# Kernel optimization log

Measured on AMD Instinct MI355X. Metric: run time of the kernel, lower is better.

## Reference

```python
import jax, jax.numpy as jnp
import numpy as np

NUM_HEADS = 12


def setup_inputs() -> dict:
    key = jax.random.key(0)
    k1, k2, k3, k4, k5 = jax.random.split(key, 5)
    B, N, C = 4, 1024, 768
    x = jax.random.normal(k1, (B, N, C), dtype=jnp.float32)
    y = jax.random.normal(k2, (B, N, C), dtype=jnp.float32)
    w_qkv = jax.random.normal(k3, (4 * C, C), dtype=jnp.float32) * 0.02
    w_proj = jax.random.normal(k4, (C, C), dtype=jnp.float32) * 0.02
    b_proj = jax.random.normal(k5, (C,), dtype=jnp.float32) * 0.02
    return {"x": x, "y": y, "w_qkv": w_qkv, "w_proj": w_proj, "b_proj": b_proj}


def reference(x, y, w_qkv, w_proj, b_proj):
    B, N, C = x.shape
    H = NUM_HEADS
    hd = C // H
    scale = hd ** (-0.5)

    def qkv4(t):
        # Linear(dim, 4*dim, bias=False): t @ W^T -> [B,N,4C] -> [4,B,H,N,hd]
        p = (t @ w_qkv.T).reshape(B, N, 4, H, hd).transpose(2, 0, 3, 1, 4)
        return p[0], p[1], p[2], p[3]

    qxo, qx, kx, vx = qkv4(x)
    qyo, qy, ky, _vy_from_y = qkv4(y)
    vy = vx  # faithful to source: vy = qkv[3] (from x), not qkv2[3]

    def attend(q, k, v, neg):
        s = jnp.einsum('bhnd,bhmd->bhnm', q, k) * scale
        a = jax.nn.softmax(-s if neg else s, axis=-1)
        o = jnp.einsum('bhnm,bhmd->bhnd', a, v)
        return o.transpose(0, 2, 1, 3).reshape(B, N, C)

    x_self = attend(qx, kx, vx, False)
    y_self = attend(qy, ky, vy, False)
    x_cross = attend(qyo, kx, vx, True)   # attnx = -(qyo @ kx^T)
    y_cross = attend(qxo, ky, vy, True)   # attny = -(qxo @ ky^T)

    out_x = (x_self + x_cross) @ w_proj.T + b_proj
    out_y = (y_self + y_cross) @ w_proj.T + b_proj
    return (out_x, out_y)
```

## Files before the change

kernel.cpp:

```cpp
#include <hip/hip_runtime.h>
#include <hip/hip_bf16.h>
#include <stdint.h>


#define BB 4
#define NN 1024
#define CC 768
#define HH 12
#define HD 64

typedef unsigned short u16;
typedef short short8 __attribute__((ext_vector_type(8)));
typedef float f32x4 __attribute__((ext_vector_type(4)));

extern "C" __device__ float __ocml_native_exp2_f32(float);

__device__ __forceinline__ u16 f2bf(float f) {
  unsigned int u = __float_as_uint(f);
  return (u16)((u + 0x7fffu + ((u >> 16) & 1u)) >> 16);
}

__device__ __forceinline__ void load_lds16(const u16* g, u16* l) {
  __builtin_amdgcn_global_load_lds((__attribute__((address_space(1))) const void*)g,
                                   (__attribute__((address_space(3))) void*)l, 16, 0, 0);
}

__global__ __launch_bounds__(256)
void cvt_bf16(const float* __restrict__ x, const float* __restrict__ y,
              const float* __restrict__ wq, const float* __restrict__ wp,
              u16* __restrict__ xb, u16* __restrict__ yb,
              u16* __restrict__ wqb, u16* __restrict__ wpb)
{
  const int seg = blockIdx.y;
  const float* src = seg == 0 ? x : (seg == 1 ? y : (seg == 2 ? wq : wp));
  u16* dst = seg == 0 ? xb : (seg == 1 ? yb : (seg == 2 ? wqb : wpb));
  const int n = (seg == 3) ? 768 * 768 : ((seg == 2) ? 3072 * 768 : 4096 * 768);
  const int i = (blockIdx.x * 256 + threadIdx.x) * 8;
  if (i >= n) return;
  float sc = 1.0f;
  if (seg == 2) {
    const int row = i / 768;
    sc = (row < 768) ? -0.18033688f : (row < 1536 ? 0.18033688f : 1.0f);
  }
  float4 a = *(const float4*)(src + i);
  float4 b = *(const float4*)(src + i + 4);
  ushort4 u0 = {f2bf(a.x * sc), f2bf(a.y * sc), f2bf(a.z * sc), f2bf(a.w * sc)};
  ushort4 u1 = {f2bf(b.x * sc), f2bf(b.y * sc), f2bf(b.z * sc), f2bf(b.w * sc)};
  *(ushort4*)(dst + i) = u0;
  *(ushort4*)(dst + i + 4) = u1;
}

__global__ __launch_bounds__(256)
void vtrans(const u16* __restrict__ qkvx, u16* __restrict__ VT)
{
  const int blk = blockIdx.x;
  const int xcd = blk & 7, slot = blk >> 3;
  const int bh = (slot >> 5) * 8 + xcd;
  const int kt = slot & 31;
  const int b = bh / HH, h = bh % HH;
  const int t = threadIdx.x;
  const int key = kt * 32 + (t >> 3), d0 = (t & 7) * 8;
  uint4 v = *(const uint4*)(qkvx + (size_t)(b * NN + key) * 3072 + 3 * CC + h * HD + d0);
  u16 e[8];
  *(uint4*)e = v;
#pragma unroll
  for (int i = 0; i < 8; i++)
    VT[(size_t)(bh * 64 + d0 + i) * 1024 + key] = e[i];
}

template<int NP, bool BF16OUT, bool BIAS>
__global__ __launch_bounds__(256)
void gemm_mfma(const u16* __restrict__ A0, const u16* __restrict__ A1,
               const u16* __restrict__ W, const float* __restrict__ bias,
               void* __restrict__ C0, void* __restrict__ C1)
{
  __shared__ u16 As[128 * 64];
  __shared__ u16 Bs[128 * 64];
  const u16* A = blockIdx.z ? A1 : A0;
  void* C = blockIdx.z ? C1 : C0;
  const int m0 = blockIdx.y * 128, n0 = blockIdx.x * 128;
  const int t = threadIdx.x, w = t >> 6, lane = t & 63;
  const int c = lane & 15, qq = lane >> 4;
  const int mq = (w >> 1) * 64, nq = (w & 1) * 64;

  const int lrow = lane >> 3;
  const int lchunk = (lane & 7) ^ lrow;
  size_t arow[4], brow[4];
#pragma unroll
  for (int i = 0; i < 4; i++) {
    const int r = (w * 4 + i) * 8 + lrow;
    arow[i] = (size_t)(m0 + r) * 768 + lchunk * 8;
    brow[i] = (size_t)(n0 + r) * 768 + lchunk * 8;
  }

  f32x4 acc[4][4] = {};
  for (int k0 = 0; k0 < 768; k0 += 64) {
    __syncthreads();
#pragma unroll
    for (int i = 0; i < 4; i++) {
      load_lds16(A + arow[i] + k0, As + (w * 4 + i) * 512);
      load_lds16(W + brow[i] + k0, Bs + (w * 4 + i) * 512);
    }
    __syncthreads();
#pragma unroll
    for (int s = 0; s < 2; s++) {
      const int swz = ((s * 4 + qq) ^ (c & 7)) * 8;
      short8 af[4], bf[4];
#pragma unroll
      for (int i = 0; i < 4; i++)
        af[i] = *(const short8*)&As[(mq + i * 16 + c) * 64 + swz];
#pragma unroll
      for (int j = 0; j < 4; j++)
        bf[j] = *(const short8*)&Bs[(nq + j * 16 + c) * 64 + swz];
#pragma unroll
      for (int i = 0; i < 4; i++)
#pragma unroll
        for (int j = 0; j < 4; j++)
          acc[i][j] = __builtin_amdgcn_mfma_f32_16x16x32_bf16(af[i], bf[j], acc[i][j], 0, 0, 0);
    }
  }
  float bj[4] = {0.f, 0.f, 0.f, 0.f};
  if (BIAS) {
#pragma unroll
    for (int j = 0; j < 4; j++) bj[j] = bias[n0 + nq + c + j * 16];
  }
#pragma unroll
  for (int i = 0; i < 4; i++)
#pragma unroll
    for (int r = 0; r < 4; r++) {
      const size_t row = (size_t)(m0 + mq + i * 16 + qq * 4 + r) * NP + n0 + nq + c;
      if (BF16OUT) {
#pragma unroll
        for (int j = 0; j < 4; j++)
          ((u16*)C)[row + j * 16] = f2bf(acc[i][j][r]);
      } else {
#pragma unroll
        for (int j = 0; j < 4; j++)
          ((float*)C)[row + j * 16] = acc[i][j][r] + bj[j];
      }
    }
}

__global__ __launch_bounds__(256, 4)
void attn_pair_mfma(const u16* __restrict__ qkvx, const u16* __restrict__ qkvy,
                    const u16* __restrict__ VT,
                    u16* __restrict__ sum_x, u16* __restrict__ sum_y)
{
  __shared__ __align__(16) u16 smem[17408];
  float (*Of)[68] = (float(*)[68])smem;

  const int blk = blockIdx.x;
  const int xcd = blk & 7, slot = blk >> 3;
  const int bh = (slot >> 5) * 8 + xcd;
  const int inner = slot & 31;
  const int qt = inner >> 1, pair = inner & 1;
  const int b = bh / HH, head = bh % HH;
  const u16* q1 = pair ? qkvy : qkvx;
  const u16* q2 = pair ? qkvx : qkvy;
  const u16* ks = pair ? qkvy : qkvx;
  u16* outp = pair ? sum_y : sum_x;

  const int t = threadIdx.x, w = t >> 6, lane = t & 63;
  const int c = lane & 15, qq = lane >> 4;

  short8 Qf[2][2];
  {
    const int qrow = qt * 64 + w * 16 + c;
    const u16* qs = q1 + (size_t)(b * NN + qrow) * 3072 + CC + head * HD + qq * 8;
    const u16* qc = q2 + (size_t)(b * NN + qrow) * 3072 + head * HD + qq * 8;
    Qf[0][0] = *(const short8*)qs;
    Qf[0][1] = *(const short8*)(qs + 32);
    Qf[1][0] = *(const short8*)qc;
    Qf[1][1] = *(const short8*)(qc + 32);
  }

  const u16* kbase = ks + (size_t)(b * NN) * 3072 + 2 * CC + head * HD;
  const u16* vtb = VT + (size_t)(bh * 64) * 1024;

  const int lr = lane >> 3;
  const int sc8 = ((lane & 7) ^ lr) * 8;

  u16* Pw = smem + 8192 + w * 2304;

  short8 ones;
#pragma unroll
  for (int i = 0; i < 8; i++) ones[i] = (short)0x3F80;

  f32x4 O[2][4] = {};
  f32x4 L[2] = {};

  const int cx = c & 7;
  const int koff0 = (qq ^ cx) * 8;
  const int koff1 = ((4 + qq) ^ cx) * 8;
  const int c6 = (6 * c) & 7;
  const int poff0 = ((qq + c6) & 7) * 8;
  const int poff1 = ((4 + qq + c6) & 7) * 8;

  for (int c16 = 0; c16 < 16; ++c16) {
    __syncthreads();
#pragma unroll
    for (int i = 0; i < 2; i++) {
      const int r = (2 * w + i) * 8 + lr;
      load_lds16(kbase + (size_t)(c16 * 64 + r) * 3072 + sc8,
                 smem + (2 * w + i) * 512);
      load_lds16(vtb + (size_t)r * 1024 + c16 * 64 + sc8,
                 smem + 4096 + (2 * w + i) * 512);
    }
    __syncthreads();

#pragma unroll
    for (int t4 = 0; t4 < 4; t4++) {
      const u16* kr = smem + (16 * t4 + c) * 64;
      short8 k0 = *(const short8*)(kr + koff0);
      short8 k1 = *(const short8*)(kr + koff1);
      const int l = 2 * t4 + (qq >> 1);
      const int base = c * 72 + (((l + c6) & 7) * 8) + 4 * (qq & 1);
#pragma unroll
      for (int s = 0; s < 2; s++) {
        f32x4 z = {0.f, 0.f, 0.f, 0.f};
        z = __builtin_amdgcn_mfma_f32_16x16x32_bf16(k0, Qf[s][0], z, 0, 0, 0);
        z = __builtin_amdgcn_mfma_f32_16x16x32_bf16(k1, Qf[s][1], z, 0, 0, 0);
        unsigned int u0 = __float_as_uint(__ocml_native_exp2_f32(z[0]));
        unsigned int u1 = __float_as_uint(__ocml_native_exp2_f32(z[1]));
        unsigned int u2 = __float_as_uint(__ocml_native_exp2_f32(z[2]));
        unsigned int u3 = __float_as_uint(__ocml_native_exp2_f32(z[3]));
        uint2 pk;
        pk.x = __builtin_amdgcn_perm(u1, u0, 0x07060302u);
        pk.y = __builtin_amdgcn_perm(u3, u2, 0x07060302u);
        *(uint2*)(Pw + s * 1152 + base) = pk;
      }
    }

    short8 pa[2][2];
#pragma unroll
    for (int s = 0; s < 2; s++) {
      const u16* pr = Pw + s * 1152 + c * 72;
      pa[s][0] = *(const short8*)(pr + poff0);
      pa[s][1] = *(const short8*)(pr + poff1);
      L[s] = __builtin_amdgcn_mfma_f32_16x16x32_bf16(pa[s][0], ones, L[s], 0, 0, 0);
      L[s] = __builtin_amdgcn_mfma_f32_16x16x32_bf16(pa[s][1], ones, L[s], 0, 0, 0);
    }
#pragma unroll
    for (int t4 = 0; t4 < 4; t4++) {
      const u16* vr = smem + 4096 + (16 * t4 + c) * 64;
      short8 v0 = *(const short8*)(vr + koff0);
      short8 v1 = *(const short8*)(vr + koff1);
#pragma unroll
      for (int s = 0; s < 2; s++) {
        O[s][t4] = __builtin_amdgcn_mfma_f32_16x16x32_bf16(pa[s][0], v0, O[s][t4], 0, 0, 0);
        O[s][t4] = __builtin_amdgcn_mfma_f32_16x16x32_bf16(pa[s][1], v1, O[s][t4], 0, 0, 0);
      }
    }
  }

  __syncthreads();
  float is[4], ic[4];
#pragma unroll
  for (int r = 0; r < 4; r++) {
    is[r] = 1.0f / L[0][r];
    ic[r] = 1.0f / L[1][r];
  }
#pragma unroll
  for (int t4 = 0; t4 < 4; t4++)
#pragma unroll
    for (int r = 0; r < 4; r++)
      Of[w * 16 + 4 * qq + r][16 * t4 + c] =
          O[0][t4][r] * is[r] + O[1][t4][r] * ic[r];
  __syncthreads();
#pragma unroll
  for (int p = 0; p < 4; p++) {
    const int idx = p * 256 + t;
    const int row = idx >> 4, c4 = (idx & 15) * 4;
    float4 v = *(const float4*)&Of[row][c4];
    ushort4 u = {f2bf(v.x), f2bf(v.y), f2bf(v.z), f2bf(v.w)};
    *(ushort4*)(outp + (size_t)(b * NN + qt * 64 + row) * CC + head * HD + c4) = u;
  }
}

extern "C" void kernel_launch(void* const* d_in, const int* in_sizes, int n_in,
                              void* d_out, int out_size, void* d_ws, size_t ws_size,
                              hipStream_t stream)
{
  const float* x      = (const float*)d_in[0];
  const float* y      = (const float*)d_in[1];
  const float* w_qkv  = (const float*)d_in[2];
  const float* w_proj = (const float*)d_in[3];
  const float* b_proj = (const float*)d_in[4];

  u16* qkv_x = (u16*)d_ws;
  u16* qkv_y = qkv_x + (size_t)4096 * 3072;
  u16* rest = qkv_y + (size_t)4096 * 3072;
  u16* sum_x = rest;
  u16* sum_y = sum_x + (size_t)4096 * 768;
  u16* x_bf  = rest;
  u16* y_bf  = x_bf + (size_t)4096 * 768;
  u16* wq_bf = y_bf + (size_t)4096 * 768;
  u16* wp_bf = wq_bf + (size_t)3072 * 768;
  u16* VT    = wp_bf + (size_t)768 * 768;
  float* out_x = (float*)d_out;
  float* out_y = out_x + (size_t)4096 * 768;

  cvt_bf16<<<dim3(1536, 4), 256, 0, stream>>>(x, y, w_qkv, w_proj,
                                              x_bf, y_bf, wq_bf, wp_bf);

  gemm_mfma<3072, true, false><<<dim3(24, 32, 2), 256, 0, stream>>>(
      x_bf, y_bf, wq_bf, nullptr, qkv_x, qkv_y);

  vtrans<<<dim3(1536), 256, 0, stream>>>(qkv_x, VT);

  attn_pair_mfma<<<dim3(1536), 256, 0, stream>>>(qkv_x, qkv_y, VT, sum_x, sum_y);

  gemm_mfma<768, false, true><<<dim3(6, 32, 2), 256, 0, stream>>>(
      sum_x, sum_y, wp_bf, b_proj, out_x, out_y);
}
```

Measured before the change: 219.5 us.

## Load K and V fragments directly from global memory, dropping LDS staging

The attention kernel no longer stages K and V tiles into shared memory with global_load_lds and block-wide barriers. Each wave now reads its MFMA operand fragments straight from global memory (through the caches), so both __syncthreads per chunk are gone. LDS use shrinks to the per-wave P buffers, and the occupancy hint rises from 4 to 5 blocks. The trade-off is that all four waves now fetch the same K/V data redundantly from global memory, with strided loads and no cross-wave reuse, which raises cache traffic and load latency.

```diff
diff --git a/kernel.cpp b/kernel.cpp
--- a/kernel.cpp
+++ b/kernel.cpp
@@ -141,12 +141,12 @@
     }
 }
 
-__global__ __launch_bounds__(256, 4)
+__global__ __launch_bounds__(256, 5)
 void attn_pair_mfma(const u16* __restrict__ qkvx, const u16* __restrict__ qkvy,
                     const u16* __restrict__ VT,
                     u16* __restrict__ sum_x, u16* __restrict__ sum_y)
 {
-  __shared__ __align__(16) u16 smem[17408];
+  __shared__ __align__(16) u16 smem[9216];
   float (*Of)[68] = (float(*)[68])smem;
 
   const int blk = blockIdx.x;
@@ -174,13 +174,10 @@
     Qf[1][1] = *(const short8*)(qc + 32);
   }
 
-  const u16* kbase = ks + (size_t)(b * NN) * 3072 + 2 * CC + head * HD;
-  const u16* vtb = VT + (size_t)(bh * 64) * 1024;
-
-  const int lr = lane >> 3;
-  const int sc8 = ((lane & 7) ^ lr) * 8;
-
-  u16* Pw = smem + 8192 + w * 2304;
+  const u16* kbase = ks + (size_t)(b * NN) * 3072 + 2 * CC + head * HD + qq * 8;
+  const u16* vbase = VT + (size_t)(bh * 64 + c) * 1024 + qq * 8;
+
+  u16* Pw = smem + w * 2304;
 
   short8 ones;
 #pragma unroll
@@ -189,30 +186,17 @@
   f32x4 O[2][4] = {};
   f32x4 L[2] = {};
 
-  const int cx = c & 7;
-  const int koff0 = (qq ^ cx) * 8;
-  const int koff1 = ((4 + qq) ^ cx) * 8;
   const int c6 = (6 * c) & 7;
   const int poff0 = ((qq + c6) & 7) * 8;
   const int poff1 = ((4 + qq + c6) & 7) * 8;
 
   for (int c16 = 0; c16 < 16; ++c16) {
-    __syncthreads();
-#pragma unroll
-    for (int i = 0; i < 2; i++) {
-      const int r = (2 * w + i) * 8 + lr;
-      load_lds16(kbase + (size_t)(c16 * 64 + r) * 3072 + sc8,
-                 smem + (2 * w + i) * 512);
-      load_lds16(vtb + (size_t)r * 1024 + c16 * 64 + sc8,
-                 smem + 4096 + (2 * w + i) * 512);
-    }
-    __syncthreads();
-
+    const u16* kt = kbase + (size_t)(c16 * 64 + c) * 3072;
 #pragma unroll
     for (int t4 = 0; t4 < 4; t4++) {
-      const u16* kr = smem + (16 * t4 + c) * 64;
-      short8 k0 = *(const short8*)(kr + koff0);
-      short8 k1 = *(const short8*)(kr + koff1);
+      const u16* kr = kt + (size_t)(16 * t4) * 3072;
+      short8 k0 = *(const short8*)kr;
+      short8 k1 = *(const short8*)(kr + 32);
       const int l = 2 * t4 + (qq >> 1);
       const int base = c * 72 + (((l + c6) & 7) * 8) + 4 * (qq & 1);
 #pragma unroll
@@ -240,11 +224,13 @@
       L[s] = __builtin_amdgcn_mfma_f32_16x16x32_bf16(pa[s][0], ones, L[s], 0, 0, 0);
       L[s] = __builtin_amdgcn_mfma_f32_16x16x32_bf16(pa[s][1], ones, L[s], 0, 0, 0);
     }
+
+    const u16* vt4 = vbase + c16 * 64;
 #pragma unroll
     for (int t4 = 0; t4 < 4; t4++) {
-      const u16* vr = smem + 4096 + (16 * t4 + c) * 64;
-      short8 v0 = *(const short8*)(vr + koff0);
-      short8 v1 = *(const short8*)(vr + koff1);
+      const u16* vr = vt4 + (size_t)(16 * t4) * 1024;
+      short8 v0 = *(const short8*)vr;
+      short8 v1 = *(const short8*)(vr + 32);
 #pragma unroll
       for (int s = 0; s < 2; s++) {
         O[s][t4] = __builtin_amdgcn_mfma_f32_16x16x32_bf16(pa[s][0], v0, O[s][t4], 0, 0, 0);
```

After: 386.1 us. 75.9% more time.

## Keep attention probabilities in registers via permuted V layout; skip unused V GEMM tiles

Applied to the files above, without the earlier changes.

The vtrans kernel now writes V^T with permuted key columns, so the P fragments produced by the QK^T MFMA output can feed the PV MFMA directly from registers. This removes the per-wave LDS round trip for P and halves the attention kernel's shared memory, and the occupancy hint rises from 4 to 5 blocks. The QKV GEMM also skips the y-side output tiles for the V columns (n >= 2304), which the reference never reads. The permutation has to line up exactly with the MFMA register layout, or results will be silently wrong.

```diff
diff --git a/kernel.cpp b/kernel.cpp
--- a/kernel.cpp
+++ b/kernel.cpp
@@ -59,16 +59,18 @@
   const int kt = slot & 31;
   const int b = bh / HH, h = bh % HH;
   const int t = threadIdx.x;
-  const int key = kt * 32 + (t >> 3), d0 = (t & 7) * 8;
+  const int kk = t >> 3;
+  const int key = kt * 32 + kk, d0 = (t & 7) * 8;
+  const int mcol = kt * 32 + ((kk >> 2) & 3) * 8 + ((kk >> 4) & 1) * 4 + (kk & 3);
   uint4 v = *(const uint4*)(qkvx + (size_t)(b * NN + key) * 3072 + 3 * CC + h * HD + d0);
   u16 e[8];
   *(uint4*)e = v;
 #pragma unroll
   for (int i = 0; i < 8; i++)
-    VT[(size_t)(bh * 64 + d0 + i) * 1024 + key] = e[i];
-}
-
-template<int NP, bool BF16OUT, bool BIAS>
+    VT[(size_t)(bh * 64 + d0 + i) * 1024 + mcol] = e[i];
+}
+
+template<int NP, bool BF16OUT, bool BIAS, int NZ1>
 __global__ __launch_bounds__(256)
 void gemm_mfma(const u16* __restrict__ A0, const u16* __restrict__ A1,
                const u16* __restrict__ W, const float* __restrict__ bias,
@@ -76,9 +78,10 @@
 {
   __shared__ u16 As[128 * 64];
   __shared__ u16 Bs[128 * 64];
+  const int m0 = blockIdx.y * 128, n0 = blockIdx.x * 128;
+  if (blockIdx.z && n0 >= NZ1) return;
   const u16* A = blockIdx.z ? A1 : A0;
   void* C = blockIdx.z ? C1 : C0;
-  const int m0 = blockIdx.y * 128, n0 = blockIdx.x * 128;
   const int t = threadIdx.x, w = t >> 6, lane = t & 63;
   const int c = lane & 15, qq = lane >> 4;
   const int mq = (w >> 1) * 64, nq = (w & 1) * 64;
@@ -141,12 +144,12 @@
     }
 }
 
-__global__ __launch_bounds__(256, 4)
+__global__ __launch_bounds__(256, 5)
 void attn_pair_mfma(const u16* __restrict__ qkvx, const u16* __restrict__ qkvy,
                     const u16* __restrict__ VT,
                     u16* __restrict__ sum_x, u16* __restrict__ sum_y)
 {
-  __shared__ __align__(16) u16 smem[17408];
+  __shared__ __align__(16) u16 smem[8704];
   float (*Of)[68] = (float(*)[68])smem;
 
   const int blk = blockIdx.x;
@@ -180,8 +183,6 @@
   const int lr = lane >> 3;
   const int sc8 = ((lane & 7) ^ lr) * 8;
 
-  u16* Pw = smem + 8192 + w * 2304;
-
   short8 ones;
 #pragma unroll
   for (int i = 0; i < 8; i++) ones[i] = (short)0x3F80;
@@ -192,9 +193,6 @@
   const int cx = c & 7;
   const int koff0 = (qq ^ cx) * 8;
   const int koff1 = ((4 + qq) ^ cx) * 8;
-  const int c6 = (6 * c) & 7;
-  const int poff0 = ((qq + c6) & 7) * 8;
-  const int poff1 = ((4 + qq + c6) & 7) * 8;
 
   for (int c16 = 0; c16 < 16; ++c16) {
     __syncthreads();
@@ -208,13 +206,12 @@
     }
     __syncthreads();
 
+    unsigned pk[2][4][2];
 #pragma unroll
     for (int t4 = 0; t4 < 4; t4++) {
       const u16* kr = smem + (16 * t4 + c) * 64;
       short8 k0 = *(const short8*)(kr + koff0);
       short8 k1 = *(const short8*)(kr + koff1);
-      const int l = 2 * t4 + (qq >> 1);
-      const int base = c * 72 + (((l + c6) & 7) * 8) + 4 * (qq & 1);
 #pragma unroll
       for (int s = 0; s < 2; s++) {
         f32x4 z = {0.f, 0.f, 0.f, 0.f};
@@ -224,22 +221,25 @@
         unsigned int u1 = __float_as_uint(__ocml_native_exp2_f32(z[1]));
         unsigned int u2 = __float_as_uint(__ocml_native_exp2_f32(z[2]));
         unsigned int u3 = __float_as_uint(__ocml_native_exp2_f32(z[3]));
-        uint2 pk;
-        pk.x = __builtin_amdgcn_perm(u1, u0, 0x07060302u);
-        pk.y = __builtin_amdgcn_perm(u3, u2, 0x07060302u);
-        *(uint2*)(Pw + s * 1152 + base) = pk;
+        pk[s][t4][0] = __builtin_amdgcn_perm(u1, u0, 0x07060302u);
+        pk[s][t4][1] = __builtin_amdgcn_perm(u3, u2, 0x07060302u);
       }
     }
 
     short8 pa[2][2];
 #pragma unroll
     for (int s = 0; s < 2; s++) {
-      const u16* pr = Pw + s * 1152 + c * 72;
-      pa[s][0] = *(const short8*)(pr + poff0);
-      pa[s][1] = *(const short8*)(pr + poff1);
+      union { unsigned u[4]; short8 s8; } f0, f1;
+      f0.u[0] = pk[s][0][0]; f0.u[1] = pk[s][0][1];
+      f0.u[2] = pk[s][1][0]; f0.u[3] = pk[s][1][1];
+      f1.u[0] = pk[s][2][0]; f1.u[1] = pk[s][2][1];
+      f1.u[2] = pk[s][3][0]; f1.u[3] = pk[s][3][1];
+      pa[s][0] = f0.s8;
+      pa[s][1] = f1.s8;
       L[s] = __builtin_amdgcn_mfma_f32_16x16x32_bf16(pa[s][0], ones, L[s], 0, 0, 0);
       L[s] = __builtin_amdgcn_mfma_f32_16x16x32_bf16(pa[s][1], ones, L[s], 0, 0, 0);
     }
+
 #pragma unroll
     for (int t4 = 0; t4 < 4; t4++) {
       const u16* vr = smem + 4096 + (16 * t4 + c) * 64;
@@ -303,13 +303,13 @@
   cvt_bf16<<<dim3(1536, 4), 256, 0, stream>>>(x, y, w_qkv, w_proj,
                                               x_bf, y_bf, wq_bf, wp_bf);
 
-  gemm_mfma<3072, true, false><<<dim3(24, 32, 2), 256, 0, stream>>>(
+  gemm_mfma<3072, true, false, 2304><<<dim3(24, 32, 2), 256, 0, stream>>>(
       x_bf, y_bf, wq_bf, nullptr, qkv_x, qkv_y);
 
   vtrans<<<dim3(1536), 256, 0, stream>>>(qkv_x, VT);
 
   attn_pair_mfma<<<dim3(1536), 256, 0, stream>>>(qkv_x, qkv_y, VT, sum_x, sum_y);
 
-  gemm_mfma<768, false, true><<<dim3(6, 32, 2), 256, 0, stream>>>(
+  gemm_mfma<768, false, true, 768><<<dim3(6, 32, 2), 256, 0, stream>>>(
       sum_x, sum_y, wp_bf, b_proj, out_x, out_y);
 }
```

Result: slower. 244.5 us (+11.4%).
